# Performance work log

Hardware: AMD Instinct MI355X
Metric: run time of the kernel (lower is better)

Reference implementation:

```python
import jax, jax.numpy as jnp
import numpy as np

DIM = 768
NUM_HEADS = 12
HEAD_DIM = DIM // NUM_HEADS
SCALE = HEAD_DIM ** -0.5


def setup_inputs() -> dict:
    key = jax.random.key(0)
    k_x, k_qkv, k_proj, k_pb = jax.random.split(key, 4)
    B, N, C = 16, 1024, DIM
    x = jax.random.normal(k_x, (B, N, C), dtype=jnp.float32)
    # qkv Linear: weight [3C, C], no bias (qkv_bias=False)
    w_qkv = jax.random.normal(k_qkv, (3 * C, C), dtype=jnp.float32) * (C ** -0.5)
    # proj Linear: weight [C, C], bias [C]
    w_proj = jax.random.normal(k_proj, (C, C), dtype=jnp.float32) * (C ** -0.5)
    b_proj = jax.random.normal(k_pb, (C,), dtype=jnp.float32) * 0.01
    return {"x": x, "w_qkv": w_qkv, "w_proj": w_proj, "b_proj": b_proj}


def reference(x, w_qkv, w_proj, b_proj):
    B, N, C = x.shape
    H, D = NUM_HEADS, HEAD_DIM
    # qkv projection: [B,N,3C] -> [3,B,H,N,D]
    qkv = jnp.einsum('bnc,ec->bne', x, w_qkv)
    qkv = qkv.reshape(B, N, 3, H, D).transpose(2, 0, 3, 1, 4)
    q, k, v = qkv[0], qkv[1], qkv[2]
    # manual attention: scores [B,H,N,N] materialized, as in source
    attn = jnp.einsum('bhqd,bhkd->bhqk', q, k) * SCALE
    attn = jax.nn.softmax(attn, axis=-1)
    out = jnp.einsum('bhqk,bhkd->bhqd', attn, v)  # [B,H,N,D]
    out = out.transpose(0, 2, 1, 3).reshape(B, N, C)
    out = jnp.einsum('bnc,oc->bno', out, w_proj) + b_proj
    return out
```

## Files before the change

kernel.cpp:

```cpp
#include <hip/hip_runtime.h>
#include <hip/hip_bf16.h>
#include <stdint.h>

typedef __attribute__((ext_vector_type(8))) short short8;
typedef __attribute__((ext_vector_type(4))) short short4v;
typedef __attribute__((ext_vector_type(4))) float floatx4;

#define B_   16
#define N_   1024
#define C_   768
#define H_   12
#define D_   64
#define K_   768
#define QSCALE 0.18033688011112042f

__device__ __forceinline__ short f2bf(float f) {
    __hip_bfloat16 h = __float2bfloat16(f);
    short s; __builtin_memcpy(&s, &h, 2); return s;
}
__device__ __forceinline__ unsigned pk2bf(float a, float b) {
    __hip_bfloat162 h = __float22bfloat162_rn(make_float2(a, b));
    unsigned u; __builtin_memcpy(&u, &h, 4); return u;
}

__device__ __forceinline__ void gl_lds16(const void* g, void* l) {
    __builtin_amdgcn_global_load_lds(
        (const __attribute__((address_space(1))) unsigned int*)g,
        (__attribute__((address_space(3))) unsigned int*)l, 16, 0, 0);
}

#define N8_X  1572864
#define N8_WQ 221184
#define N8_WP 73728
__global__ void cvt_all(const float* __restrict__ x, const float* __restrict__ wq,
                        const float* __restrict__ wp, short* __restrict__ xb,
                        short* __restrict__ wqb, short* __restrict__ wpb)
{
    long i = (long)blockIdx.x * 256 + threadIdx.x;
    const float* src; short* dst;
    if (i < N8_X)              { src = x;  dst = xb;  }
    else if (i < N8_X + N8_WQ) { src = wq; dst = wqb; i -= N8_X; }
    else                       { src = wp; dst = wpb; i -= (long)N8_X + N8_WQ; }
    const float4* p = (const float4*)src + 2 * i;
    const float4 u = p[0], v = p[1];
    short8 r;
    r[0] = f2bf(u.x); r[1] = f2bf(u.y); r[2] = f2bf(u.z); r[3] = f2bf(u.w);
    r[4] = f2bf(v.x); r[5] = f2bf(v.y); r[6] = f2bf(v.z); r[7] = f2bf(v.w);
    *((short8*)dst + i) = r;
}

template<int MODE>
__global__ __launch_bounds__(256, 3)
void gemm_bt(const short* __restrict__ A, const short* __restrict__ Bm,
             const float* __restrict__ bias,
             short* __restrict__ q_ws, short* __restrict__ k_ws,
             short* __restrict__ v_ws, float* __restrict__ outp)
{
    __shared__ short Alds[128 * 32];
    __shared__ short Blds[128 * 32];
    const int tid  = threadIdx.x;
    const int wave = tid >> 6, lane = tid & 63;
    const int cl   = lane & 15, quad = lane >> 4;
    const int bm = blockIdx.x, bn = blockIdx.y;
    const int wm = (wave >> 1) * 64, wn = (wave & 1) * 64;

    const short* Ag = A  + (long)bm * 128 * K_ + (long)(tid >> 2) * K_ + (tid & 3) * 8;
    const short* Bg = Bm + (long)bn * 128 * K_ + (long)(tid >> 2) * K_ + (tid & 3) * 8;
    short* la = Alds + (tid & 0xC0) * 8;
    short* lb = Blds + (tid & 0xC0) * 8;

    const floatx4 fzero = {0.f, 0.f, 0.f, 0.f};
    floatx4 acc[4][4];
    #pragma unroll
    for (int i = 0; i < 4; i++)
        #pragma unroll
        for (int j = 0; j < 4; j++) acc[i][j] = fzero;

    for (int kt = 0; kt < K_; kt += 32) {
        __syncthreads();
        gl_lds16(Ag + kt,            la);
        gl_lds16(Ag + kt + 64 * K_,  la + 2048);
        gl_lds16(Bg + kt,            lb);
        gl_lds16(Bg + kt + 64 * K_,  lb + 2048);
        __syncthreads();

        short8 af[4], bf[4];
        #pragma unroll
        for (int i = 0; i < 4; i++)
            af[i] = *(const short8*)(Alds + (wm + i * 16 + cl) * 32 + quad * 8);
        #pragma unroll
        for (int j = 0; j < 4; j++)
            bf[j] = *(const short8*)(Blds + (wn + j * 16 + cl) * 32 + quad * 8);
        #pragma unroll
        for (int i = 0; i < 4; i++)
            #pragma unroll
            for (int j = 0; j < 4; j++)
                acc[i][j] = __builtin_amdgcn_mfma_f32_16x16x32_bf16(af[i], bf[j], acc[i][j], 0, 0, 0);
    }

    #pragma unroll
    for (int i = 0; i < 4; i++) {
        const int gm0 = bm * 128 + wm + i * 16 + quad * 4;
        #pragma unroll
        for (int j = 0; j < 4; j++) {
            const int gn = bn * 128 + wn + j * 16 + cl;
            if (MODE == 0) {
                const int t   = bn / 6;
                const int rem = gn - t * 768;
                const int h   = rem >> 6, d = rem & 63;
                const int b   = gm0 >> 10;
                const int n0  = gm0 & 1023;
                const int bh  = b * H_ + h;
                if (t == 2) {
                    short4v pk;
                    #pragma unroll
                    for (int r = 0; r < 4; r++) pk[r] = f2bf(acc[i][j][r]);
                    *(short4v*)(v_ws + (((long)(bh * D_ + d)) << 10) + n0) = pk;
                } else {
                    short* dst = (t == 0) ? q_ws : k_ws;
                    const float sc = (t == 0) ? QSCALE : 1.0f;
                    #pragma unroll
                    for (int r = 0; r < 4; r++)
                        dst[((long)bh * N_ + (n0 + r)) * D_ + d] = f2bf(acc[i][j][r] * sc);
                }
            } else {
                const float bv = bias[gn];
                #pragma unroll
                for (int r = 0; r < 4; r++)
                    outp[(long)(gm0 + r) * C_ + gn] = acc[i][j][r] + bv;
            }
        }
    }
}

__global__ __launch_bounds__(256, 3)
void attn_fused(const short* __restrict__ q_ws, const short* __restrict__ k_ws,
                const short* __restrict__ v_ws, short* __restrict__ o_ws)
{
    __shared__ short Klds[128 * 64];
    __shared__ short Vlds[64 * 128];
    __shared__ short Plds[4][16 * 136];

    const int tid  = threadIdx.x;
    const int wave = tid >> 6, lane = tid & 63;
    const int cl   = lane & 15, quad = lane >> 4;

    const int linear = blockIdx.y * 8 + blockIdx.x;
    const int xcd = linear & 7, slot = linear >> 3;
    const int bh  = xcd * 24 + (slot >> 3);
    const int qt  = slot & 7;

    const long base = (long)bh * (N_ * D_);
    const int  qr0  = qt * 128 + wave * 32 + cl;

    short8 qf[2][2];
    #pragma unroll
    for (int mt = 0; mt < 2; mt++) {
        qf[mt][0] = *(const short8*)(q_ws + base + (long)(qr0 + mt * 16) * D_ + quad * 8);
        qf[mt][1] = *(const short8*)(q_ws + base + (long)(qr0 + mt * 16) * D_ + 32 + quad * 8);
    }

    const floatx4 fzero = {0.f, 0.f, 0.f, 0.f};
    float m_r[2][4], l_r[2][4];
    floatx4 o_acc[2][4];
    #pragma unroll
    for (int mt = 0; mt < 2; mt++)
        #pragma unroll
        for (int r = 0; r < 4; r++) {
            m_r[mt][r] = -1e30f; l_r[mt][r] = 0.f; o_acc[mt][r] = fzero;
        }

    const int skey = tid >> 3, sseg = tid & 7;
    const int vd   = tid >> 4, vseg = tid & 15;
    short* pl = &Plds[wave][0];

    for (int kc = 0; kc < N_; kc += 128) {
        short8 kst[4], vst[4];
        #pragma unroll
        for (int p = 0; p < 4; p++) {
            kst[p] = *(const short8*)(k_ws + base + (long)(kc + p * 32 + skey) * D_ + sseg * 8);
            vst[p] = *(const short8*)(v_ws + base + (long)(p * 16 + vd) * N_ + kc + vseg * 8);
        }
        __syncthreads();
        #pragma unroll
        for (int p = 0; p < 4; p++) {
            const int krow = p * 32 + skey;
            const int fk   = ((krow >> 3) ^ (krow & 7)) & 7;
            *(short8*)(Klds + krow * 64 + (sseg ^ fk) * 8) = kst[p];
            const int vrow = p * 16 + vd;
            *(short8*)(Vlds + vrow * 128 + (vseg ^ (vrow & 7)) * 8) = vst[p];
        }
        __syncthreads();

        floatx4 s[2][8];
        #pragma unroll
        for (int nt = 0; nt < 8; nt++) {
            const int krow = cl * 8 + nt;
            const int fk   = ((krow >> 3) ^ (krow & 7)) & 7;
            const short* kr = Klds + krow * 64;
            short8 kf0 = *(const short8*)(kr + ((quad    ) ^ fk) * 8);
            short8 kf1 = *(const short8*)(kr + ((quad + 4) ^ fk) * 8);
            floatx4 t0 = fzero, t1 = fzero;
            t0 = __builtin_amdgcn_mfma_f32_16x16x32_bf16(qf[0][0], kf0, t0, 0, 0, 0);
            t0 = __builtin_amdgcn_mfma_f32_16x16x32_bf16(qf[0][1], kf1, t0, 0, 0, 0);
            t1 = __builtin_amdgcn_mfma_f32_16x16x32_bf16(qf[1][0], kf0, t1, 0, 0, 0);
            t1 = __builtin_amdgcn_mfma_f32_16x16x32_bf16(qf[1][1], kf1, t1, 0, 0, 0);
            s[0][nt] = t0; s[1][nt] = t1;
        }

        #pragma unroll
        for (int mt = 0; mt < 2; mt++) {
            float alpha[4];
            #pragma unroll
            for (int r = 0; r < 4; r++) {
                float v = fmaxf(fmaxf(s[mt][0][r], s[mt][1][r]), fmaxf(s[mt][2][r], s[mt][3][r]));
                v = fmaxf(v, fmaxf(fmaxf(s[mt][4][r], s[mt][5][r]), fmaxf(s[mt][6][r], s[mt][7][r])));
                v = fmaxf(v, __shfl_xor(v, 1));
                v = fmaxf(v, __shfl_xor(v, 2));
                v = fmaxf(v, __shfl_xor(v, 4));
                v = fmaxf(v, __shfl_xor(v, 8));
                const float mn = fmaxf(m_r[mt][r], v);
                alpha[r] = __builtin_amdgcn_exp2f(m_r[mt][r] - mn);
                m_r[mt][r] = mn;
                l_r[mt][r] *= alpha[r];
            }
            #pragma unroll
            for (int r = 0; r < 4; r++) {
                float p0 = __builtin_amdgcn_exp2f(s[mt][0][r] - m_r[mt][r]);
                float p1 = __builtin_amdgcn_exp2f(s[mt][1][r] - m_r[mt][r]);
                float p2 = __builtin_amdgcn_exp2f(s[mt][2][r] - m_r[mt][r]);
                float p3 = __builtin_amdgcn_exp2f(s[mt][3][r] - m_r[mt][r]);
                float p4 = __builtin_amdgcn_exp2f(s[mt][4][r] - m_r[mt][r]);
                float p5 = __builtin_amdgcn_exp2f(s[mt][5][r] - m_r[mt][r]);
                float p6 = __builtin_amdgcn_exp2f(s[mt][6][r] - m_r[mt][r]);
                float p7 = __builtin_amdgcn_exp2f(s[mt][7][r] - m_r[mt][r]);
                l_r[mt][r] += ((p0 + p1) + (p2 + p3)) + ((p4 + p5) + (p6 + p7));
                uint4 pk = { pk2bf(p0, p1), pk2bf(p2, p3), pk2bf(p4, p5), pk2bf(p6, p7) };
                *(uint4*)(pl + (quad * 4 + r) * 136 + cl * 8) = pk;
            }
            #pragma unroll
            for (int dt = 0; dt < 4; dt++) {
                o_acc[mt][dt][0] *= alpha[0]; o_acc[mt][dt][1] *= alpha[1];
                o_acc[mt][dt][2] *= alpha[2]; o_acc[mt][dt][3] *= alpha[3];
            }
            asm volatile("" ::: "memory");

            #pragma unroll
            for (int ks = 0; ks < 4; ks++) {
                short8 pf = *(const short8*)(pl + cl * 136 + ks * 32 + quad * 8);
                #pragma unroll
                for (int dt = 0; dt < 4; dt++) {
                    const int vrow = dt * 16 + cl;
                    const short* vr = Vlds + vrow * 128;
                    short8 vf = *(const short8*)(vr + ((ks * 4 + quad) ^ (vrow & 7)) * 8);
                    o_acc[mt][dt] = __builtin_amdgcn_mfma_f32_16x16x32_bf16(pf, vf, o_acc[mt][dt], 0, 0, 0);
                }
            }
            asm volatile("" ::: "memory");
        }
    }

    const int b = bh / H_, h = bh - b * H_;
    #pragma unroll
    for (int mt = 0; mt < 2; mt++) {
        #pragma unroll
        for (int r = 0; r < 4; r++) {
            float v = l_r[mt][r];
            v += __shfl_xor(v, 1); v += __shfl_xor(v, 2);
            v += __shfl_xor(v, 4); v += __shfl_xor(v, 8);
            l_r[mt][r] = 1.0f / v;
        }
        const int nrow = qt * 128 + wave * 32 + mt * 16 + quad * 4;
        #pragma unroll
        for (int dt = 0; dt < 4; dt++) {
            const int c = h * D_ + dt * 16 + cl;
            #pragma unroll
            for (int r = 0; r < 4; r++)
                o_ws[((long)(b * N_ + nrow + r)) * C_ + c] = f2bf(o_acc[mt][dt][r] * l_r[mt][r]);
        }
    }
}

extern "C" void kernel_launch(void* const* d_in, const int* in_sizes, int n_in,
                              void* d_out, int out_size, void* d_ws, size_t ws_size,
                              hipStream_t stream)
{
    const float* x      = (const float*)d_in[0];
    const float* w_qkv  = (const float*)d_in[1];
    const float* w_proj = (const float*)d_in[2];
    const float* b_proj = (const float*)d_in[3];
    float* out = (float*)d_out;

    const long SZ = (long)B_ * N_ * C_;
    short* q_ws   = (short*)d_ws;
    short* k_ws   = q_ws + SZ;
    short* v_ws   = k_ws + SZ;
    short* x_bf   = v_ws + SZ;
    short* o_ws   = x_bf;
    short* wqkv_bf  = x_bf + SZ;
    short* wproj_bf = wqkv_bf + (long)3 * C_ * C_;

    cvt_all<<<dim3(7296), 256, 0, stream>>>(x, w_qkv, w_proj, x_bf, wqkv_bf, wproj_bf);
    gemm_bt<0><<<dim3(128, 18), 256, 0, stream>>>(x_bf, wqkv_bf, nullptr, q_ws, k_ws, v_ws, nullptr);
    attn_fused<<<dim3(8, 192), 256, 0, stream>>>(q_ws, k_ws, v_ws, o_ws);
    gemm_bt<1><<<dim3(128, 6), 256, 0, stream>>>(o_ws, wproj_bf, b_proj, nullptr, nullptr, nullptr, out);
}
```

Measured before the change: 304.1 us.

## Alias softmax P buffer into K LDS tile and raise occupancy to four blocks

Stores the bf16 probability tile in the K shared-memory region instead of a separate buffer, adding a barrier after score computation so K reads finish first. The P layout switches from a padded stride to an XOR-swizzled stride of 128. Launch bounds are raised to four blocks per CU, and exponentials are computed in place in registers before the barrier. A dummy padding array is kept alive via a never-taken branch to fix the LDS footprint. The tighter register budget and extra barrier may cause spills or stalls.

```diff
diff --git a/kernel.cpp b/kernel.cpp
--- a/kernel.cpp
+++ b/kernel.cpp
@@ -133,13 +133,13 @@
     }
 }
 
-__global__ __launch_bounds__(256, 3)
+__global__ __launch_bounds__(256, 4)
 void attn_fused(const short* __restrict__ q_ws, const short* __restrict__ k_ws,
                 const short* __restrict__ v_ws, short* __restrict__ o_ws)
 {
     __shared__ short Klds[128 * 64];
     __shared__ short Vlds[64 * 128];
-    __shared__ short Plds[4][16 * 136];
+    __shared__ short lds_pad[4096];
 
     const int tid  = threadIdx.x;
     const int wave = tid >> 6, lane = tid & 63;
@@ -149,6 +149,7 @@
     const int xcd = linear & 7, slot = linear >> 3;
     const int bh  = xcd * 24 + (slot >> 3);
     const int qt  = slot & 7;
+    if ((int)blockIdx.z == 1) o_ws[0] = lds_pad[tid];
 
     const long base = (long)bh * (N_ * D_);
     const int  qr0  = qt * 128 + wave * 32 + cl;
@@ -172,7 +173,7 @@
 
     const int skey = tid >> 3, sseg = tid & 7;
     const int vd   = tid >> 4, vseg = tid & 15;
-    short* pl = &Plds[wave][0];
+    short* pl = Klds + wave * 2048;
 
     for (int kc = 0; kc < N_; kc += 128) {
         short8 kst[4], vst[4];
@@ -208,9 +209,9 @@
             s[0][nt] = t0; s[1][nt] = t1;
         }
 
+        float alpha[2][4];
         #pragma unroll
         for (int mt = 0; mt < 2; mt++) {
-            float alpha[4];
             #pragma unroll
             for (int r = 0; r < 4; r++) {
                 float v = fmaxf(fmaxf(s[mt][0][r], s[mt][1][r]), fmaxf(s[mt][2][r], s[mt][3][r]));
@@ -220,34 +221,39 @@
                 v = fmaxf(v, __shfl_xor(v, 4));
                 v = fmaxf(v, __shfl_xor(v, 8));
                 const float mn = fmaxf(m_r[mt][r], v);
-                alpha[r] = __builtin_amdgcn_exp2f(m_r[mt][r] - mn);
+                alpha[mt][r] = __builtin_amdgcn_exp2f(m_r[mt][r] - mn);
                 m_r[mt][r] = mn;
-                l_r[mt][r] *= alpha[r];
-            }
+                float lsum = l_r[mt][r] * alpha[mt][r];
+                #pragma unroll
+                for (int nt = 0; nt < 8; nt++) {
+                    const float p = __builtin_amdgcn_exp2f(s[mt][nt][r] - mn);
+                    s[mt][nt][r] = p;
+                    lsum += p;
+                }
+                l_r[mt][r] = lsum;
+            }
+        }
+        __syncthreads();
+
+        #pragma unroll
+        for (int mt = 0; mt < 2; mt++) {
             #pragma unroll
             for (int r = 0; r < 4; r++) {
-                float p0 = __builtin_amdgcn_exp2f(s[mt][0][r] - m_r[mt][r]);
-                float p1 = __builtin_amdgcn_exp2f(s[mt][1][r] - m_r[mt][r]);
-                float p2 = __builtin_amdgcn_exp2f(s[mt][2][r] - m_r[mt][r]);
-                float p3 = __builtin_amdgcn_exp2f(s[mt][3][r] - m_r[mt][r]);
-                float p4 = __builtin_amdgcn_exp2f(s[mt][4][r] - m_r[mt][r]);
-                float p5 = __builtin_amdgcn_exp2f(s[mt][5][r] - m_r[mt][r]);
-                float p6 = __builtin_amdgcn_exp2f(s[mt][6][r] - m_r[mt][r]);
-                float p7 = __builtin_amdgcn_exp2f(s[mt][7][r] - m_r[mt][r]);
-                l_r[mt][r] += ((p0 + p1) + (p2 + p3)) + ((p4 + p5) + (p6 + p7));
-                uint4 pk = { pk2bf(p0, p1), pk2bf(p2, p3), pk2bf(p4, p5), pk2bf(p6, p7) };
-                *(uint4*)(pl + (quad * 4 + r) * 136 + cl * 8) = pk;
+                const int pr = quad * 4 + r;
+                uint4 pk = { pk2bf(s[mt][0][r], s[mt][1][r]), pk2bf(s[mt][2][r], s[mt][3][r]),
+                             pk2bf(s[mt][4][r], s[mt][5][r]), pk2bf(s[mt][6][r], s[mt][7][r]) };
+                *(uint4*)(pl + pr * 128 + ((cl ^ (pr & 7)) * 8)) = pk;
             }
             #pragma unroll
             for (int dt = 0; dt < 4; dt++) {
-                o_acc[mt][dt][0] *= alpha[0]; o_acc[mt][dt][1] *= alpha[1];
-                o_acc[mt][dt][2] *= alpha[2]; o_acc[mt][dt][3] *= alpha[3];
+                o_acc[mt][dt][0] *= alpha[mt][0]; o_acc[mt][dt][1] *= alpha[mt][1];
+                o_acc[mt][dt][2] *= alpha[mt][2]; o_acc[mt][dt][3] *= alpha[mt][3];
             }
             asm volatile("" ::: "memory");
 
             #pragma unroll
             for (int ks = 0; ks < 4; ks++) {
-                short8 pf = *(const short8*)(pl + cl * 136 + ks * 32 + quad * 8);
+                short8 pf = *(const short8*)(pl + cl * 128 + (((ks * 4 + quad) ^ (cl & 7)) * 8));
                 #pragma unroll
                 for (int dt = 0; dt < 4; dt++) {
                     const int vrow = dt * 16 + cl;
```

Result: slower. 445.6 us (+46.5%).
